# Kernel optimization log

Measured on AMD Instinct MI355X. Metric: run time of the kernel, lower is better.

Reference implementation:

```python
import jax, jax.numpy as jnp
import numpy as np

N = 65536      # total points (single batch, multiple of patch_size)
C = 512        # channels
H = 8          # heads
K = 256        # patch (window) size
SCALE = 0.125  # head_dim ** -0.5


def setup_inputs() -> dict:
    key = jax.random.key(0)
    k1, k2, k3, k4 = jax.random.split(key, 4)
    feat = jax.random.normal(k1, (N, C), dtype=jnp.float32)
    # serialized order = permutation of points; inverse undoes it
    order = jax.random.permutation(k2, N).astype(jnp.int64)
    inverse = jnp.argsort(order).astype(jnp.int64)
    Wqkv = jax.random.normal(k3, (C, 3 * C), dtype=jnp.float32) * (C ** -0.5)
    bqkv = jnp.zeros((3 * C,), dtype=jnp.float32)
    Wproj = jax.random.normal(k4, (C, C), dtype=jnp.float32) * (C ** -0.5)
    bproj = jnp.zeros((C,), dtype=jnp.float32)
    return {"feat": feat, "order": order, "inverse": inverse,
            "Wqkv": Wqkv, "bqkv": bqkv, "Wproj": Wproj, "bproj": bproj}


def reference(feat, order, inverse, Wqkv, bqkv, Wproj, bproj):
    d = C // H
    P = N // K  # number of windows
    # QKV projection then gather into serialized patch order
    qkv = feat @ Wqkv + bqkv                    # [N, 3C]
    qkv = qkv[order].reshape(P, K, 3, H, d)     # [P, K, 3, H, d]
    q, k, v = qkv[:, :, 0], qkv[:, :, 1], qkv[:, :, 2]  # each [P, K, H, d]
    # windowed attention within each patch
    scores = jnp.einsum("pkhd,pmhd->phkm", q, k) * SCALE  # [P, H, K, K]
    attn = jax.nn.softmax(scores, axis=-1)
    out = jnp.einsum("phkm,pmhd->pkhd", attn, v)          # [P, K, H, d]
    out = out.reshape(N, C)[inverse]                       # unpad / de-serialize
    return out @ Wproj + bproj
```

## Files before the change

kernel.cpp:

```cpp
#include <hip/hip_runtime.h>
#include <stdint.h>

#define N_TOK 65536
#define CDIM  512
#define C3    1536
#define HEADS 8
#define DHEAD 64
#define KTOK  256
#define PGRP  256

typedef __attribute__((ext_vector_type(8))) short bf16x8;
typedef __attribute__((ext_vector_type(4))) float f32x4;
typedef __attribute__((ext_vector_type(16))) float f32x16;
typedef __attribute__((ext_vector_type(4))) unsigned u32x4;

__device__ __forceinline__ unsigned short f2bf(float f) {
  union { float f; unsigned u; } t; t.f = f;
  return (unsigned short)((t.u + 0x7fffu + ((t.u >> 16) & 1u)) >> 16);
}

__device__ __forceinline__ unsigned cvt_pk_bf16(float lo, float hi) {
  unsigned r;
  asm("v_cvt_pk_bf16_f32 %0, %1, %2" : "=v"(r) : "v"(lo), "v"(hi));
  return r;
}

__global__ __launch_bounds__(256) void prep_k(const float* __restrict__ feat,
                                              unsigned short* __restrict__ featb,
                                              const float* __restrict__ Wqkv,
                                              unsigned short* __restrict__ wqkvT,
                                              const float* __restrict__ Wproj,
                                              unsigned short* __restrict__ wprojT) {
  __shared__ float tile[32][33];
  int bid = blockIdx.x;
  if (bid < 4096) {
    size_t stride = (size_t)4096 * 256 * 4;
    size_t base = ((size_t)bid * 256 + threadIdx.x) * 4;
#pragma unroll
    for (int it = 0; it < 8; ++it) {
      size_t i = base + (size_t)it * stride;
      float4 v = *(const float4*)(feat + i);
      ushort4 o;
      o.x = f2bf(v.x); o.y = f2bf(v.y); o.z = f2bf(v.z); o.w = f2bf(v.w);
      *(ushort4*)(featb + i) = o;
    }
  } else {
    const float* in; unsigned short* out; int Cc, bx, by;
    if (bid < 4096 + 768) {
      int r = bid - 4096; in = Wqkv; out = wqkvT; Cc = C3; bx = r % 48; by = r / 48;
    } else {
      int r = bid - (4096 + 768); in = Wproj; out = wprojT; Cc = CDIM; bx = r % 16; by = r / 16;
    }
    int c0 = bx * 32, r0 = by * 32;
    int tx = threadIdx.x & 31, ty = threadIdx.x >> 5;
    for (int i = ty; i < 32; i += 8)
      tile[i][tx] = in[(size_t)(r0 + i) * Cc + c0 + tx];
    __syncthreads();
    for (int i = ty; i < 32; i += 8)
      out[(size_t)(c0 + i) * CDIM + r0 + tx] = f2bf(tile[tx][i]);
  }
}

template <int OF32>
__global__ __launch_bounds__(512, 2) void gemm256(const unsigned short* __restrict__ A,
                                                  const unsigned short* __restrict__ Bt,
                                                  const float* __restrict__ bias,
                                                  void* __restrict__ Cout,
                                                  const int* __restrict__ gather,
                                                  int Nn, int Kk, int nbn) {
  __shared__ __align__(16) unsigned short As[2][256 * 64];
  __shared__ __align__(16) unsigned short Bs[2][256 * 64];

  int cpx = gridDim.x >> 3;
  int wk = (blockIdx.x & 7) * cpx + (blockIdx.x >> 3);
  int bm = wk / nbn, bn = wk % nbn;
  int m0 = bm * 256, n0 = bn * 256;

  int tid = threadIdx.x;
  int wv = tid >> 6, ln = tid & 63, g = ln >> 4, c = ln & 15;
  int wr = wv >> 2, wc = wv & 3;
  int NT = Kk >> 6;

  const char* Ab = (const char*)A;
  const char* Bb = (const char*)Bt;
  int lr = tid >> 3;
  int cg = (tid & 7) ^ (lr & 7);
  unsigned aoff[2][2], boff[2][2];
#pragma unroll
  for (int h2 = 0; h2 < 2; ++h2)
#pragma unroll
    for (int j = 0; j < 2; ++j) {
      int row = h2 * 128 + j * 64 + lr;
      int ga = gather ? gather[m0 + row] : (m0 + row);
      aoff[h2][j] = (unsigned)(((size_t)ga * Kk + cg * 8) * 2);
      boff[h2][j] = (unsigned)(((size_t)(n0 + row) * Kk + cg * 8) * 2);
    }

#define STAGE_A(t, h2) do { int _s = (t) & 1; unsigned _k = (unsigned)(t) * 128u;             \
    __builtin_amdgcn_global_load_lds(                                                          \
        (__attribute__((address_space(1))) void*)(void*)(Ab + aoff[h2][0] + _k),               \
        (__attribute__((address_space(3))) void*)&As[_s][((h2) * 1024 + wv * 64) * 8],         \
        16, 0, 0);                                                                             \
    __builtin_amdgcn_global_load_lds(                                                          \
        (__attribute__((address_space(1))) void*)(void*)(Ab + aoff[h2][1] + _k),               \
        (__attribute__((address_space(3))) void*)&As[_s][((h2) * 1024 + 512 + wv * 64) * 8],   \
        16, 0, 0);                                                                             \
  } while (0)
#define STAGE_B(t, h2) do { int _s = (t) & 1; unsigned _k = (unsigned)(t) * 128u;             \
    __builtin_amdgcn_global_load_lds(                                                          \
        (__attribute__((address_space(1))) void*)(void*)(Bb + boff[h2][0] + _k),               \
        (__attribute__((address_space(3))) void*)&Bs[_s][((h2) * 1024 + wv * 64) * 8],         \
        16, 0, 0);                                                                             \
    __builtin_amdgcn_global_load_lds(                                                          \
        (__attribute__((address_space(1))) void*)(void*)(Bb + boff[h2][1] + _k),               \
        (__attribute__((address_space(3))) void*)&Bs[_s][((h2) * 1024 + 512 + wv * 64) * 8],   \
        16, 0, 0);                                                                             \
  } while (0)
#define RD_A(mi, kc) (*(const bf16x8*)&Ac[((((2 * (mi) + wr) * 16 + c) * 8 + (((kc) * 4 + g) ^ (c & 7))) * 8)])
#define RD_B(ni, kc) (*(const bf16x8*)&Bc[((((4 * (ni) + wc) * 16 + c) * 8 + (((kc) * 4 + g) ^ (c & 7))) * 8)])

  f32x4 acc[8][4];
#pragma unroll
  for (int mi = 0; mi < 8; ++mi)
#pragma unroll
    for (int ni = 0; ni < 4; ++ni)
      acc[mi][ni] = (f32x4){0.f, 0.f, 0.f, 0.f};

  STAGE_A(0, 0); STAGE_A(0, 1); STAGE_B(0, 0); STAGE_B(0, 1);
  STAGE_A(1, 0); STAGE_A(1, 1); STAGE_B(1, 0); STAGE_B(1, 1);
  asm volatile("s_waitcnt vmcnt(8)" ::: "memory");
  __builtin_amdgcn_s_barrier();

  bf16x8 af[4][2], bf[2][2];

#pragma unroll 1
  for (int v = 0; v < NT; ++v) {
    unsigned short* Ac = &As[v & 1][0];
    unsigned short* Bc = &Bs[v & 1][0];

#pragma unroll
    for (int i = 0; i < 4; ++i)
#pragma unroll
      for (int kc = 0; kc < 2; ++kc) af[i][kc] = RD_A(i, kc);
#pragma unroll
    for (int j = 0; j < 2; ++j)
#pragma unroll
      for (int kc = 0; kc < 2; ++kc) bf[j][kc] = RD_B(j, kc);
    if (v >= 1 && v + 1 < NT) STAGE_A(v + 1, 1);
    __builtin_amdgcn_s_barrier();
    asm volatile("s_waitcnt lgkmcnt(0)" ::: "memory");
    __builtin_amdgcn_sched_barrier(0);
    __builtin_amdgcn_s_setprio(1);
#pragma unroll
    for (int i = 0; i < 4; ++i)
#pragma unroll
      for (int j = 0; j < 2; ++j) {
        acc[i][j] = __builtin_amdgcn_mfma_f32_16x16x32_bf16(af[i][0], bf[j][0], acc[i][j], 0, 0, 0);
        acc[i][j] = __builtin_amdgcn_mfma_f32_16x16x32_bf16(af[i][1], bf[j][1], acc[i][j], 0, 0, 0);
      }
    __builtin_amdgcn_s_setprio(0);
    __builtin_amdgcn_s_barrier();

#pragma unroll
    for (int j = 0; j < 2; ++j)
#pragma unroll
      for (int kc = 0; kc < 2; ++kc) bf[j][kc] = RD_B(2 + j, kc);
    if (v >= 1 && v + 1 < NT) STAGE_B(v + 1, 0);
    __builtin_amdgcn_s_barrier();
    asm volatile("s_waitcnt lgkmcnt(0)" ::: "memory");
    __builtin_amdgcn_sched_barrier(0);
    __builtin_amdgcn_s_setprio(1);
#pragma unroll
    for (int i = 0; i < 4; ++i)
#pragma unroll
      for (int j = 0; j < 2; ++j) {
        acc[i][2 + j] = __builtin_amdgcn_mfma_f32_16x16x32_bf16(af[i][0], bf[j][0], acc[i][2 + j], 0, 0, 0);
        acc[i][2 + j] = __builtin_amdgcn_mfma_f32_16x16x32_bf16(af[i][1], bf[j][1], acc[i][2 + j], 0, 0, 0);
      }
    __builtin_amdgcn_s_setprio(0);
    __builtin_amdgcn_s_barrier();

#pragma unroll
    for (int i = 0; i < 4; ++i)
#pragma unroll
      for (int kc = 0; kc < 2; ++kc) af[i][kc] = RD_A(4 + i, kc);
    if (v + 2 < NT) STAGE_A(v + 2, 0);
    __builtin_amdgcn_s_barrier();
    asm volatile("s_waitcnt lgkmcnt(0)" ::: "memory");
    __builtin_amdgcn_sched_barrier(0);
    __builtin_amdgcn_s_setprio(1);
#pragma unroll
    for (int i = 0; i < 4; ++i)
#pragma unroll
      for (int j = 0; j < 2; ++j) {
        acc[4 + i][2 + j] = __builtin_amdgcn_mfma_f32_16x16x32_bf16(af[i][0], bf[j][0], acc[4 + i][2 + j], 0, 0, 0);
        acc[4 + i][2 + j] = __builtin_amdgcn_mfma_f32_16x16x32_bf16(af[i][1], bf[j][1], acc[4 + i][2 + j], 0, 0, 0);
      }
    __builtin_amdgcn_s_setprio(0);
    __builtin_amdgcn_s_barrier();

#pragma unroll
    for (int j = 0; j < 2; ++j)
#pragma unroll
      for (int kc = 0; kc < 2; ++kc) bf[j][kc] = RD_B(j, kc);
    if (v + 2 < NT) STAGE_B(v + 2, 1);
    __builtin_amdgcn_s_barrier();
    asm volatile("s_waitcnt lgkmcnt(0)" ::: "memory");
    __builtin_amdgcn_sched_barrier(0);
    __builtin_amdgcn_s_setprio(1);
#pragma unroll
    for (int i = 0; i < 4; ++i)
#pragma unroll
      for (int j = 0; j < 2; ++j) {
        acc[4 + i][j] = __builtin_amdgcn_mfma_f32_16x16x32_bf16(af[i][0], bf[j][0], acc[4 + i][j], 0, 0, 0);
        acc[4 + i][j] = __builtin_amdgcn_mfma_f32_16x16x32_bf16(af[i][1], bf[j][1], acc[4 + i][j], 0, 0, 0);
      }
    __builtin_amdgcn_s_setprio(0);
    if (v + 2 < NT) asm volatile("s_waitcnt vmcnt(4)" ::: "memory");
    else            asm volatile("s_waitcnt vmcnt(0)" ::: "memory");
    __builtin_amdgcn_s_barrier();
  }

#pragma unroll
  for (int ni = 0; ni < 4; ++ni) {
    int col = n0 + (4 * ni + wc) * 16 + c;
    float bv = bias[col];
#pragma unroll
    for (int mi = 0; mi < 8; ++mi) {
      int rowb = m0 + (2 * mi + wr) * 16 + g * 4;
#pragma unroll
      for (int rr = 0; rr < 4; ++rr) {
        float vv = acc[mi][ni][rr] + bv;
        if (OF32) ((float*)Cout)[(size_t)(rowb + rr) * Nn + col] = vv;
        else ((unsigned short*)Cout)[(size_t)(rowb + rr) * Nn + col] = f2bf(vv);
      }
    }
  }
#undef STAGE_A
#undef STAGE_B
#undef RD_A
#undef RD_B
}

__global__ __launch_bounds__(256, 2) void attn_k(const unsigned short* __restrict__ qkv,
                                                 const int* __restrict__ order,
                                                 unsigned short* __restrict__ attnout) {
  __shared__ __align__(16) unsigned short Ks[KTOK * 64];
  __shared__ __align__(16) unsigned short Vt[64 * 256];

  int p = blockIdx.x >> 3, h = blockIdx.x & 7;
  int tid = threadIdx.x;
  int wv = tid >> 6, ln = tid & 63;
  int lq = ln & 31;
  int hl = ln >> 5;

  const unsigned short* base = qkv + (size_t)p * KTOK * C3 + h * DHEAD;

  {
    int mlo = tid >> 3;
    int j = (tid & 7) ^ (mlo & 7);
    const unsigned short* ksrc = base + CDIM + j * 8;
#pragma unroll
    for (int i = 0; i < 8; ++i) {
      int m = i * 32 + mlo;
      __builtin_amdgcn_global_load_lds(
          (const __attribute__((address_space(1))) void*)(ksrc + (size_t)m * C3),
          (__attribute__((address_space(3))) void*)&Ks[((i << 8) + tid) * 8],
          16, 0, 0);
    }
  }
  {
    const unsigned short* vrow = base + 2 * CDIM + (size_t)tid * C3;
    bf16x8 vv[8];
#pragma unroll
    for (int j = 0; j < 8; ++j) vv[j] = *(const bf16x8*)(vrow + j * 8);
#pragma unroll
    for (int j = 0; j < 8; ++j)
#pragma unroll
      for (int e = 0; e < 8; ++e) {
        int d = j * 8 + e;
        Vt[d * 256 + (((tid >> 3) ^ (d & 7)) << 3) + (tid & 7)] = (unsigned short)vv[j][e];
      }
  }

  bf16x8 qfa[2][4];
  {
    const unsigned short* qr = base + (size_t)(wv * 64 + lq) * C3;
#pragma unroll
    for (int dk = 0; dk < 4; ++dk) qfa[0][dk] = *(const bf16x8*)(qr + dk * 16 + hl * 8);
  }
  __syncthreads();

#pragma unroll
  for (int t = 0; t < 2; ++t) {
    int q0 = wv * 64 + t * 32;
    int ordv[16];
#pragma unroll
    for (int r = 0; r < 16; ++r)
      ordv[r] = order[p * KTOK + q0 + (r & 3) + 8 * (r >> 2) + 4 * hl];

    f32x16 sa[8];
    __builtin_amdgcn_s_setprio(1);
#pragma unroll
    for (int mt = 0; mt < 8; ++mt) {
      f32x16 z;
#pragma unroll
      for (int r = 0; r < 16; ++r) z[r] = 0.f;
      int m = mt * 32 + lq;
#pragma unroll
      for (int dk = 0; dk < 4; ++dk) {
        bf16x8 kf = *(const bf16x8*)&Ks[(m * 8 + ((dk * 2 + hl) ^ (m & 7))) * 8];
        z = __builtin_amdgcn_mfma_f32_32x32x16_bf16(kf, qfa[t][dk], z, 0, 0, 0);
      }
      sa[mt] = z;
    }
    __builtin_amdgcn_s_setprio(0);

    if (t == 0) {
      const unsigned short* qr = base + (size_t)(wv * 64 + 32 + lq) * C3;
#pragma unroll
      for (int dk = 0; dk < 4; ++dk) qfa[1][dk] = *(const bf16x8*)(qr + dk * 16 + hl * 8);
    }

    float mx = sa[0][0];
#pragma unroll
    for (int mt = 0; mt < 8; ++mt)
#pragma unroll
      for (int r = 0; r < 16; ++r) mx = fmaxf(mx, sa[mt][r]);
    mx = fmaxf(mx, __shfl_xor(mx, 32, 64));
    float sum = 0.f;
#pragma unroll
    for (int mt = 0; mt < 8; ++mt)
#pragma unroll
      for (int r = 0; r < 16; ++r) {
        float e = __expf((sa[mt][r] - mx) * 0.125f);
        sa[mt][r] = e;
        sum += e;
      }
    sum += __shfl_xor(sum, 32, 64);
    float inv = 1.f / sum;

    f32x16 oa[2];
#pragma unroll
    for (int r = 0; r < 16; ++r) { oa[0][r] = 0.f; oa[1][r] = 0.f; }
#pragma unroll
    for (int kt = 0; kt < 16; ++kt) {
      int mt = kt >> 1, rb = (kt & 1) * 8;
      unsigned L0 = cvt_pk_bf16(sa[mt][rb + 0] * inv, sa[mt][rb + 1] * inv);
      unsigned L1 = cvt_pk_bf16(sa[mt][rb + 2] * inv, sa[mt][rb + 3] * inv);
      unsigned H0 = cvt_pk_bf16(sa[mt][rb + 4] * inv, sa[mt][rb + 5] * inv);
      unsigned H1 = cvt_pk_bf16(sa[mt][rb + 6] * inv, sa[mt][rb + 7] * inv);
      auto s0 = __builtin_amdgcn_permlane32_swap(L0, H0, false, false);
      auto s1 = __builtin_amdgcn_permlane32_swap(L1, H1, false, false);
      u32x4 pw;
      pw[0] = s0[0]; pw[1] = s1[0]; pw[2] = s0[1]; pw[3] = s1[1];
      bf16x8 pf = __builtin_bit_cast(bf16x8, pw);
      __builtin_amdgcn_s_setprio(1);
#pragma unroll
      for (int dt = 0; dt < 2; ++dt) {
        int d = dt * 32 + lq;
        bf16x8 vf = *(const bf16x8*)&Vt[(d * 32 + ((kt * 2 + hl) ^ (d & 7))) * 8];
        oa[dt] = __builtin_amdgcn_mfma_f32_32x32x16_bf16(pf, vf, oa[dt], 0, 0, 0);
      }
      __builtin_amdgcn_s_setprio(0);
    }

    size_t cb = (size_t)h * DHEAD + lq;
#pragma unroll
    for (int r = 0; r < 16; ++r) {
      size_t rb2 = (size_t)ordv[r] * CDIM + cb;
      attnout[rb2] = f2bf(oa[0][r]);
      attnout[rb2 + 32] = f2bf(oa[1][r]);
    }
  }
}

extern "C" void kernel_launch(void* const* d_in, const int* in_sizes, int n_in,
                              void* d_out, int out_size, void* d_ws, size_t ws_size,
                              hipStream_t stream) {
  const float* feat  = (const float*)d_in[0];
  const int*   order = (const int*)d_in[1];
  const float* Wqkv  = (const float*)d_in[3];
  const float* bqkv  = (const float*)d_in[4];
  const float* Wproj = (const float*)d_in[5];
  const float* bproj = (const float*)d_in[6];
  float* out = (float*)d_out;

  char* ws = (char*)d_ws;
  unsigned short* qkv    = (unsigned short*)ws;
  unsigned short* featb  = (unsigned short*)(ws + (size_t)N_TOK * C3 * 2);
  unsigned short* attn   = featb;
  unsigned short* wqkvT  = (unsigned short*)(ws + (size_t)N_TOK * C3 * 2 + (size_t)N_TOK * CDIM * 2);
  unsigned short* wprojT = wqkvT + C3 * CDIM;

  prep_k<<<4096 + 768 + 256, 256, 0, stream>>>(feat, featb, Wqkv, wqkvT, Wproj, wprojT);

  gemm256<0><<<(N_TOK / 256) * (C3 / 256), 512, 0, stream>>>(
      featb, wqkvT, bqkv, qkv, order, C3, CDIM, C3 / 256);

  attn_k<<<PGRP * HEADS, 256, 0, stream>>>(qkv, order, attn);

  gemm256<1><<<(N_TOK / 256) * (CDIM / 256), 512, 0, stream>>>(
      attn, wprojT, bproj, out, nullptr, CDIM, CDIM, CDIM / 256);
}
```

Baseline: 505.3 us.

## Software-pipeline LDS fragment reads across MFMA phases with double register buffers

Reorders the GEMM main loop so shared-memory fragment reads for the next sub-tile overlap the MFMA work of the current one. It uses separate LO/HI register fragment sets and partial lgkmcnt waits instead of full drains. The first A/B fragments of the next K-tile are prefetched at the end of each iteration. This is meant to hide LDS read latency behind matrix instructions, at the cost of more VGPR pressure. The prefetch also reads the next buffer before the closing barrier, so data loaded by other waves may not be visible yet.

Result: slower. 563.4 us (+11.5%).

```diff
diff --git a/kernel.cpp b/kernel.cpp
--- a/kernel.cpp
+++ b/kernel.cpp
@@ -116,8 +116,8 @@
         (__attribute__((address_space(3))) void*)&Bs[_s][((h2) * 1024 + 512 + wv * 64) * 8],   \
         16, 0, 0);                                                                             \
   } while (0)
-#define RD_A(mi, kc) (*(const bf16x8*)&Ac[((((2 * (mi) + wr) * 16 + c) * 8 + (((kc) * 4 + g) ^ (c & 7))) * 8)])
-#define RD_B(ni, kc) (*(const bf16x8*)&Bc[((((4 * (ni) + wc) * 16 + c) * 8 + (((kc) * 4 + g) ^ (c & 7))) * 8)])
+#define RD_A(P, mi, kc) (*(const bf16x8*)&(P)[((((2 * (mi) + wr) * 16 + c) * 8 + (((kc) * 4 + g) ^ (c & 7))) * 8)])
+#define RD_B(P, ni, kc) (*(const bf16x8*)&(P)[((((4 * (ni) + wc) * 16 + c) * 8 + (((kc) * 4 + g) ^ (c & 7))) * 8)])
 
   f32x4 acc[8][4];
 #pragma unroll
@@ -131,22 +131,66 @@
   asm volatile("s_waitcnt vmcnt(8)" ::: "memory");
   __builtin_amdgcn_s_barrier();
 
-  bf16x8 af[4][2], bf[2][2];
+  bf16x8 afLO[4][2], afHI[4][2], bfLO[2][2], bfHI[2][2];
+  {
+    unsigned short* Ac = &As[0][0];
+    unsigned short* Bc = &Bs[0][0];
+#pragma unroll
+    for (int i = 0; i < 4; ++i)
+#pragma unroll
+      for (int kc = 0; kc < 2; ++kc) afLO[i][kc] = RD_A(Ac, i, kc);
+#pragma unroll
+    for (int j = 0; j < 2; ++j)
+#pragma unroll
+      for (int kc = 0; kc < 2; ++kc) bfLO[j][kc] = RD_B(Bc, j, kc);
+  }
 
 #pragma unroll 1
   for (int v = 0; v < NT; ++v) {
     unsigned short* Ac = &As[v & 1][0];
     unsigned short* Bc = &Bs[v & 1][0];
-
-#pragma unroll
-    for (int i = 0; i < 4; ++i)
-#pragma unroll
-      for (int kc = 0; kc < 2; ++kc) af[i][kc] = RD_A(i, kc);
+    unsigned short* An2 = &As[(v + 1) & 1][0];
+    unsigned short* Bn2 = &Bs[(v + 1) & 1][0];
+
 #pragma unroll
     for (int j = 0; j < 2; ++j)
 #pragma unroll
-      for (int kc = 0; kc < 2; ++kc) bf[j][kc] = RD_B(j, kc);
+      for (int kc = 0; kc < 2; ++kc) bfHI[j][kc] = RD_B(Bc, 2 + j, kc);
     if (v >= 1 && v + 1 < NT) STAGE_A(v + 1, 1);
+    __builtin_amdgcn_s_barrier();
+    asm volatile("s_waitcnt lgkmcnt(4)" ::: "memory");
+    __builtin_amdgcn_sched_barrier(0);
+    __builtin_amdgcn_s_setprio(1);
+#pragma unroll
+    for (int i = 0; i < 4; ++i)
+#pragma unroll
+      for (int j = 0; j < 2; ++j) {
+        acc[i][j] = __builtin_amdgcn_mfma_f32_16x16x32_bf16(afLO[i][0], bfLO[j][0], acc[i][j], 0, 0, 0);
+        acc[i][j] = __builtin_amdgcn_mfma_f32_16x16x32_bf16(afLO[i][1], bfLO[j][1], acc[i][j], 0, 0, 0);
+      }
+    __builtin_amdgcn_s_setprio(0);
+    __builtin_amdgcn_s_barrier();
+
+#pragma unroll
+    for (int i = 0; i < 4; ++i)
+#pragma unroll
+      for (int kc = 0; kc < 2; ++kc) afHI[i][kc] = RD_A(Ac, 4 + i, kc);
+    if (v >= 1 && v + 1 < NT) STAGE_B(v + 1, 0);
+    __builtin_amdgcn_s_barrier();
+    asm volatile("s_waitcnt lgkmcnt(8)" ::: "memory");
+    __builtin_amdgcn_sched_barrier(0);
+    __builtin_amdgcn_s_setprio(1);
+#pragma unroll
+    for (int i = 0; i < 4; ++i)
+#pragma unroll
+      for (int j = 0; j < 2; ++j) {
+        acc[i][2 + j] = __builtin_amdgcn_mfma_f32_16x16x32_bf16(afLO[i][0], bfHI[j][0], acc[i][2 + j], 0, 0, 0);
+        acc[i][2 + j] = __builtin_amdgcn_mfma_f32_16x16x32_bf16(afLO[i][1], bfHI[j][1], acc[i][2 + j], 0, 0, 0);
+      }
+    __builtin_amdgcn_s_setprio(0);
+    __builtin_amdgcn_s_barrier();
+
+    if (v + 2 < NT) STAGE_A(v + 2, 0);
     __builtin_amdgcn_s_barrier();
     asm volatile("s_waitcnt lgkmcnt(0)" ::: "memory");
     __builtin_amdgcn_sched_barrier(0);
@@ -155,69 +199,36 @@
     for (int i = 0; i < 4; ++i)
 #pragma unroll
       for (int j = 0; j < 2; ++j) {
-        acc[i][j] = __builtin_amdgcn_mfma_f32_16x16x32_bf16(af[i][0], bf[j][0], acc[i][j], 0, 0, 0);
-        acc[i][j] = __builtin_amdgcn_mfma_f32_16x16x32_bf16(af[i][1], bf[j][1], acc[i][j], 0, 0, 0);
+        acc[4 + i][2 + j] = __builtin_amdgcn_mfma_f32_16x16x32_bf16(afHI[i][0], bfHI[j][0], acc[4 + i][2 + j], 0, 0, 0);
+        acc[4 + i][2 + j] = __builtin_amdgcn_mfma_f32_16x16x32_bf16(afHI[i][1], bfHI[j][1], acc[4 + i][2 + j], 0, 0, 0);
       }
     __builtin_amdgcn_s_setprio(0);
     __builtin_amdgcn_s_barrier();
 
-#pragma unroll
-    for (int j = 0; j < 2; ++j)
-#pragma unroll
-      for (int kc = 0; kc < 2; ++kc) bf[j][kc] = RD_B(2 + j, kc);
-    if (v >= 1 && v + 1 < NT) STAGE_B(v + 1, 0);
-    __builtin_amdgcn_s_barrier();
-    asm volatile("s_waitcnt lgkmcnt(0)" ::: "memory");
+    if (v + 2 < NT) STAGE_B(v + 2, 1);
+    __builtin_amdgcn_s_barrier();
     __builtin_amdgcn_sched_barrier(0);
     __builtin_amdgcn_s_setprio(1);
 #pragma unroll
     for (int i = 0; i < 4; ++i)
 #pragma unroll
       for (int j = 0; j < 2; ++j) {
-        acc[i][2 + j] = __builtin_amdgcn_mfma_f32_16x16x32_bf16(af[i][0], bf[j][0], acc[i][2 + j], 0, 0, 0);
-        acc[i][2 + j] = __builtin_amdgcn_mfma_f32_16x16x32_bf16(af[i][1], bf[j][1], acc[i][2 + j], 0, 0, 0);
-      }
-    __builtin_amdgcn_s_setprio(0);
-    __builtin_amdgcn_s_barrier();
-
-#pragma unroll
-    for (int i = 0; i < 4; ++i)
-#pragma unroll
-      for (int kc = 0; kc < 2; ++kc) af[i][kc] = RD_A(4 + i, kc);
-    if (v + 2 < NT) STAGE_A(v + 2, 0);
-    __builtin_amdgcn_s_barrier();
-    asm volatile("s_waitcnt lgkmcnt(0)" ::: "memory");
-    __builtin_amdgcn_sched_barrier(0);
-    __builtin_amdgcn_s_setprio(1);
-#pragma unroll
-    for (int i = 0; i < 4; ++i)
-#pragma unroll
-      for (int j = 0; j < 2; ++j) {
-        acc[4 + i][2 + j] = __builtin_amdgcn_mfma_f32_16x16x32_bf16(af[i][0], bf[j][0], acc[4 + i][2 + j], 0, 0, 0);
-        acc[4 + i][2 + j] = __builtin_amdgcn_mfma_f32_16x16x32_bf16(af[i][1], bf[j][1], acc[4 + i][2 + j], 0, 0, 0);
-      }
-    __builtin_amdgcn_s_setprio(0);
-    __builtin_amdgcn_s_barrier();
-
-#pragma unroll
-    for (int j = 0; j < 2; ++j)
-#pragma unroll
-      for (int kc = 0; kc < 2; ++kc) bf[j][kc] = RD_B(j, kc);
-    if (v + 2 < NT) STAGE_B(v + 2, 1);
-    __builtin_amdgcn_s_barrier();
-    asm volatile("s_waitcnt lgkmcnt(0)" ::: "memory");
-    __builtin_amdgcn_sched_barrier(0);
-    __builtin_amdgcn_s_setprio(1);
-#pragma unroll
-    for (int i = 0; i < 4; ++i)
-#pragma unroll
-      for (int j = 0; j < 2; ++j) {
-        acc[4 + i][j] = __builtin_amdgcn_mfma_f32_16x16x32_bf16(af[i][0], bf[j][0], acc[4 + i][j], 0, 0, 0);
-        acc[4 + i][j] = __builtin_amdgcn_mfma_f32_16x16x32_bf16(af[i][1], bf[j][1], acc[4 + i][j], 0, 0, 0);
+        acc[4 + i][j] = __builtin_amdgcn_mfma_f32_16x16x32_bf16(afHI[i][0], bfLO[j][0], acc[4 + i][j], 0, 0, 0);
+        acc[4 + i][j] = __builtin_amdgcn_mfma_f32_16x16x32_bf16(afHI[i][1], bfLO[j][1], acc[4 + i][j], 0, 0, 0);
       }
     __builtin_amdgcn_s_setprio(0);
     if (v + 2 < NT) asm volatile("s_waitcnt vmcnt(4)" ::: "memory");
     else            asm volatile("s_waitcnt vmcnt(0)" ::: "memory");
+    if (v + 1 < NT) {
+#pragma unroll
+      for (int i = 0; i < 4; ++i)
+#pragma unroll
+        for (int kc = 0; kc < 2; ++kc) afLO[i][kc] = RD_A(An2, i, kc);
+#pragma unroll
+      for (int j = 0; j < 2; ++j)
+#pragma unroll
+        for (int kc = 0; kc < 2; ++kc) bfLO[j][kc] = RD_B(Bn2, j, kc);
+    }
     __builtin_amdgcn_s_barrier();
   }
 
```
